# Kernel optimization log

Hardware: AMD Instinct MI355X
Metric: run time of the kernel (lower is better)

## Reference

```python
import jax, jax.numpy as jnp
import numpy as np

B, N, D, S = 4, 8, 64, 8192  # batch, heads, dim_head, seq_len


def setup_inputs() -> dict:
    key = jax.random.key(0)
    kq, kk, kv = jax.random.split(key, 3)
    q = jax.random.normal(kq, (B, N, D, S), dtype=jnp.float32)
    k = jax.random.normal(kk, (B, N, D, S), dtype=jnp.float32)
    v = jax.random.normal(kv, (B, N, D, S), dtype=jnp.float32)
    return {"q": q, "k": k, "v": v}


def reference(q, k, v):
    # q, k, v: [b, n, d, s] = [batch, heads, dim_head, seq]
    scale = q.shape[-2] ** -0.5  # dim_head^-0.5
    qs = jax.nn.softmax(q, axis=-2) * scale   # softmax over feature dim
    ks = jax.nn.softmax(k, axis=-1)           # softmax over seq dim
    # kv context: [b, n, d, d] -- avoids the O(s^2) score matrix
    context = jnp.einsum('bnis,bnjs->bnij', ks, v)
    # out: [b, n, d, s]
    return jnp.einsum('bnij,bnis->bnjs', context, qs)
```

## Files before the change

kernel.cpp:

```cpp
#include <hip/hip_runtime.h>
#include <math.h>


typedef _Float16 half8 __attribute__((ext_vector_type(8)));
typedef float floatx4 __attribute__((ext_vector_type(4)));
typedef float floatx16 __attribute__((ext_vector_type(16)));

constexpr int BHEADS = 32;
constexpr int DH     = 64;
constexpr int SEQ    = 8192;
constexpr int NCHUNK = 32;
constexpr float QSCALE = 0.125f;

__global__ __launch_bounds__(256)
void ctx_partial_kernel(const float* __restrict__ K, const float* __restrict__ V,
                        float* __restrict__ partial, float* __restrict__ Zp)
{
    const int head  = blockIdx.y;
    const int chunk = blockIdx.x;
    const int t     = threadIdx.x;
    const int lane  = t & 63;
    const int w     = t >> 6;
    const int ln    = lane & 15;
    const int q8    = lane >> 4;

    const float* kh = K + (size_t)head * DH * SEQ;
    const float* vh = V + (size_t)head * DH * SEQ;

    __shared__ __align__(16) _Float16 et[64 * 72];
    __shared__ __align__(16) _Float16 vt[64 * 72];
    __shared__ __align__(16) float zred[64 * 8];

    const int r0 = t >> 3;
    const int c0 = 8 * (t & 7);
    const int s_blk = chunk * 256;

    float4 pk[2][2], pv[2][2];
    #pragma unroll
    for (int rr = 0; rr < 2; ++rr) {
        const size_t base = (size_t)(r0 + 32 * rr) * SEQ + s_blk + c0;
        pk[rr][0] = *(const float4*)(kh + base);
        pk[rr][1] = *(const float4*)(kh + base + 4);
        pv[rr][0] = *(const float4*)(vh + base);
        pv[rr][1] = *(const float4*)(vh + base + 4);
    }

    floatx4 acc[4];
    #pragma unroll
    for (int jt = 0; jt < 4; ++jt) acc[jt] = (floatx4){0.f, 0.f, 0.f, 0.f};
    float zacc[2] = {0.f, 0.f};

    for (int ts = 0; ts < 4; ++ts) {
        #pragma unroll
        for (int rr = 0; rr < 2; ++rr) {
            const int row = r0 + 32 * rr;
            float e[8];
            e[0] = __expf(pk[rr][0].x); e[1] = __expf(pk[rr][0].y);
            e[2] = __expf(pk[rr][0].z); e[3] = __expf(pk[rr][0].w);
            e[4] = __expf(pk[rr][1].x); e[5] = __expf(pk[rr][1].y);
            e[6] = __expf(pk[rr][1].z); e[7] = __expf(pk[rr][1].w);
            zacc[rr] += e[0]+e[1]+e[2]+e[3]+e[4]+e[5]+e[6]+e[7];
            half8 he, hv;
            #pragma unroll
            for (int x = 0; x < 4; ++x) {
                he[x] = (_Float16)e[x]; he[x+4] = (_Float16)e[x+4];
            }
            hv[0] = (_Float16)pv[rr][0].x; hv[1] = (_Float16)pv[rr][0].y;
            hv[2] = (_Float16)pv[rr][0].z; hv[3] = (_Float16)pv[rr][0].w;
            hv[4] = (_Float16)pv[rr][1].x; hv[5] = (_Float16)pv[rr][1].y;
            hv[6] = (_Float16)pv[rr][1].z; hv[7] = (_Float16)pv[rr][1].w;
            *(half8*)(et + row * 72 + c0) = he;
            *(half8*)(vt + row * 72 + c0) = hv;
        }
        if (ts < 3) {
            #pragma unroll
            for (int rr = 0; rr < 2; ++rr) {
                const size_t base = (size_t)(r0 + 32 * rr) * SEQ + s_blk
                                    + (ts + 1) * 64 + c0;
                pk[rr][0] = *(const float4*)(kh + base);
                pk[rr][1] = *(const float4*)(kh + base + 4);
                pv[rr][0] = *(const float4*)(vh + base);
                pv[rr][1] = *(const float4*)(vh + base + 4);
            }
        }
        __syncthreads();
        #pragma unroll
        for (int st = 0; st < 2; ++st) {
            const half8 a = *(const half8*)(et + (16 * w + ln) * 72 + st * 32 + q8 * 8);
            #pragma unroll
            for (int jt = 0; jt < 4; ++jt) {
                const half8 b = *(const half8*)(vt + (16 * jt + ln) * 72 + st * 32 + q8 * 8);
                acc[jt] = __builtin_amdgcn_mfma_f32_16x16x32_f16(a, b, acc[jt], 0, 0, 0);
            }
        }
        __syncthreads();
    }

    float* ph = partial + (size_t)(head * NCHUNK + chunk) * DH * DH;
    #pragma unroll
    for (int jt = 0; jt < 4; ++jt) {
        #pragma unroll
        for (int rr = 0; rr < 4; ++rr) {
            const int i = 16 * w + q8 * 4 + rr;
            const int j = 16 * jt + ln;
            ph[i * DH + j] = acc[jt][rr];
        }
    }
    zred[r0 * 8 + (t & 7)] = zacc[0];
    zred[(r0 + 32) * 8 + (t & 7)] = zacc[1];
    __syncthreads();
    if (t < 64) {
        const float4 z0 = *(const float4*)(zred + t * 8);
        const float4 z1 = *(const float4*)(zred + t * 8 + 4);
        Zp[(head * NCHUNK + chunk) * DH + t] =
            z0.x + z0.y + z0.z + z0.w + z1.x + z1.y + z1.z + z1.w;
    }
}

__global__ __launch_bounds__(256)
void reduce_kernel(const float* __restrict__ partial, const float* __restrict__ Zp,
                   _Float16* __restrict__ czT)
{
    const int h  = blockIdx.x >> 2;
    const int iq = blockIdx.x & 3;
    const int t  = threadIdx.x;
    __shared__ float rz[16];

    if (t < 16) {
        float z = 0.f;
        #pragma unroll
        for (int c = 0; c < NCHUNK; ++c)
            z += Zp[(h * NCHUNK + c) * DH + 16 * iq + t];
        rz[t] = 1.0f / z;
    }
    __syncthreads();

    const int il = t >> 4;
    const int j4 = t & 15;
    const int i  = 16 * iq + il;
    const float* ph = partial + (size_t)h * NCHUNK * DH * DH;
    float4 sum = {0.f, 0.f, 0.f, 0.f};
    #pragma unroll
    for (int c = 0; c < NCHUNK; ++c) {
        const float4 p = *(const float4*)(ph + (size_t)c * DH * DH + i * DH + j4 * 4);
        sum.x += p.x; sum.y += p.y; sum.z += p.z; sum.w += p.w;
    }
    const float r = rz[il];
    _Float16* ct = czT + (size_t)h * DH * DH;
    ct[(j4 * 4 + 0) * DH + i] = (_Float16)(sum.x * r);
    ct[(j4 * 4 + 1) * DH + i] = (_Float16)(sum.y * r);
    ct[(j4 * 4 + 2) * DH + i] = (_Float16)(sum.z * r);
    ct[(j4 * 4 + 3) * DH + i] = (_Float16)(sum.w * r);
}

__global__ __launch_bounds__(256)
void out_kernel(const float* __restrict__ Q, const _Float16* __restrict__ czT,
                float* __restrict__ out)
{
    const int head = blockIdx.y;
    const int sb   = blockIdx.x;
    const int t    = threadIdx.x;
    const int lane = t & 63;
    const int w    = t >> 6;
    const int l31  = lane & 31;
    const int lh   = lane >> 5;
    const int jw   = 32 * (w & 1);
    const int sw   = 32 * (w >> 1);

    __shared__ __align__(16) float    qf[64 * 68];
    __shared__ __align__(16) _Float16 eqT[64 * 64];
    __shared__ __align__(16) float    wred[64 * 4];

    const float* qh = Q + (size_t)head * DH * SEQ;
    const int r0 = t >> 4;
    const int sc = 4 * (t & 15);
    const int s0 = sb * 128;

    float4 pq[4];
    #pragma unroll
    for (int p = 0; p < 4; ++p)
        pq[p] = *(const float4*)(qh + (size_t)(r0 + 16 * p) * SEQ + s0 + sc);

    const _Float16* ch = czT + (size_t)head * DH * DH;
    half8 afr[4];
    #pragma unroll
    for (int st = 0; st < 4; ++st)
        afr[st] = *(const half8*)(ch + (jw + l31) * DH + st * 16 + lh * 8);

    for (int r = 0; r < 2; ++r) {
        #pragma unroll
        for (int p = 0; p < 4; ++p)
            *(float4*)(qf + (r0 + 16 * p) * 68 + sc) = pq[p];
        if (r < 1) {
            #pragma unroll
            for (int p = 0; p < 4; ++p)
                pq[p] = *(const float4*)(qh + (size_t)(r0 + 16 * p) * SEQ
                                         + s0 + 64 + sc);
        }
        __syncthreads();
        {
            const int s  = t & 63;
            const int cg = t >> 6;
            float wsum = 0.f;
            #pragma unroll
            for (int h2 = 0; h2 < 2; ++h2) {
                const int cc = cg + 4 * h2;
                half8 p8;
                #pragma unroll
                for (int jj = 0; jj < 8; ++jj) {
                    const float e = __expf(qf[(8 * cc + jj) * 68 + s]);
                    wsum += e;
                    p8[jj] = (_Float16)e;
                }
                *(half8*)(eqT + s * 64 + ((cc ^ (s & 7)) * 8)) = p8;
            }
            wred[s * 4 + cg] = wsum;
        }
        __syncthreads();
        const float4 wv = *(const float4*)(wred + (sw + l31) * 4);
        const float rw = QSCALE / (wv.x + wv.y + wv.z + wv.w);
        floatx16 acc = {};
        #pragma unroll
        for (int st = 0; st < 4; ++st) {
            const int s2 = sw + l31;
            const int cc = 2 * st + lh;
            const half8 b = *(const half8*)(eqT + s2 * 64 + ((cc ^ (s2 & 7)) * 8));
            acc = __builtin_amdgcn_mfma_f32_32x32x16_f16(afr[st], b, acc, 0, 0, 0);
        }
        float* oh = out + (size_t)head * DH * SEQ + s0 + r * 64;
        #pragma unroll
        for (int rg = 0; rg < 16; ++rg) {
            const int j = jw + (rg & 3) + 8 * (rg >> 2) + 4 * lh;
            oh[(size_t)j * SEQ + sw + l31] = acc[rg] * rw;
        }
    }
}

extern "C" void kernel_launch(void* const* d_in, const int* in_sizes, int n_in,
                              void* d_out, int out_size, void* d_ws, size_t ws_size,
                              hipStream_t stream)
{
    const float* q = (const float*)d_in[0];
    const float* k = (const float*)d_in[1];
    const float* v = (const float*)d_in[2];
    float* out = (float*)d_out;

    float*    partial = (float*)d_ws;
    float*    Zp      = partial + BHEADS * NCHUNK * DH * DH;
    _Float16* czT     = (_Float16*)(Zp + BHEADS * NCHUNK * DH);

    ctx_partial_kernel<<<dim3(NCHUNK, BHEADS), 256, 0, stream>>>(k, v, partial, Zp);
    reduce_kernel<<<BHEADS * 4, 256, 0, stream>>>(partial, Zp, czT);
    out_kernel<<<dim3(64, BHEADS), 256, 0, stream>>>(q, czT, out);
}
```

Before: 237.8 us.

## Load MFMA operands directly from global memory, drop LDS staging in ctx kernel

The context-partial kernel no longer stages exp(K) and V through shared memory with barriers. Each lane loads its MFMA fragment straight from global memory into registers, double-buffered across 8 k-steps, and converts to fp16 in registers. Per-row Z sums now use wave shuffles instead of an LDS reduction. The reduce kernel is split into 4x more blocks with one scalar output per thread, and every thread recomputes its Z sum. In exchange, each V fragment is loaded redundantly by all 4 waves and the global accesses are less coalesced (32-byte segments per row).

```diff
diff --git a/kernel.cpp b/kernel.cpp
--- a/kernel.cpp
+++ b/kernel.cpp
@@ -24,76 +24,60 @@
     const int ln    = lane & 15;
     const int q8    = lane >> 4;
 
-    const float* kh = K + (size_t)head * DH * SEQ;
-    const float* vh = V + (size_t)head * DH * SEQ;
-
-    __shared__ __align__(16) _Float16 et[64 * 72];
-    __shared__ __align__(16) _Float16 vt[64 * 72];
-    __shared__ __align__(16) float zred[64 * 8];
-
-    const int r0 = t >> 3;
-    const int c0 = 8 * (t & 7);
-    const int s_blk = chunk * 256;
-
-    float4 pk[2][2], pv[2][2];
-    #pragma unroll
-    for (int rr = 0; rr < 2; ++rr) {
-        const size_t base = (size_t)(r0 + 32 * rr) * SEQ + s_blk + c0;
-        pk[rr][0] = *(const float4*)(kh + base);
-        pk[rr][1] = *(const float4*)(kh + base + 4);
-        pv[rr][0] = *(const float4*)(vh + base);
-        pv[rr][1] = *(const float4*)(vh + base + 4);
-    }
+    const int s0 = chunk * 256;
+    const float* ka = K + (size_t)head * DH * SEQ
+                        + (size_t)(16 * w + ln) * SEQ + s0 + q8 * 8;
+    const float* va = V + (size_t)head * DH * SEQ
+                        + (size_t)ln * SEQ + s0 + q8 * 8;
 
     floatx4 acc[4];
     #pragma unroll
     for (int jt = 0; jt < 4; ++jt) acc[jt] = (floatx4){0.f, 0.f, 0.f, 0.f};
-    float zacc[2] = {0.f, 0.f};
-
-    for (int ts = 0; ts < 4; ++ts) {
-        #pragma unroll
-        for (int rr = 0; rr < 2; ++rr) {
-            const int row = r0 + 32 * rr;
-            float e[8];
-            e[0] = __expf(pk[rr][0].x); e[1] = __expf(pk[rr][0].y);
-            e[2] = __expf(pk[rr][0].z); e[3] = __expf(pk[rr][0].w);
-            e[4] = __expf(pk[rr][1].x); e[5] = __expf(pk[rr][1].y);
-            e[6] = __expf(pk[rr][1].z); e[7] = __expf(pk[rr][1].w);
-            zacc[rr] += e[0]+e[1]+e[2]+e[3]+e[4]+e[5]+e[6]+e[7];
-            half8 he, hv;
-            #pragma unroll
-            for (int x = 0; x < 4; ++x) {
-                he[x] = (_Float16)e[x]; he[x+4] = (_Float16)e[x+4];
-            }
-            hv[0] = (_Float16)pv[rr][0].x; hv[1] = (_Float16)pv[rr][0].y;
-            hv[2] = (_Float16)pv[rr][0].z; hv[3] = (_Float16)pv[rr][0].w;
-            hv[4] = (_Float16)pv[rr][1].x; hv[5] = (_Float16)pv[rr][1].y;
-            hv[6] = (_Float16)pv[rr][1].z; hv[7] = (_Float16)pv[rr][1].w;
-            *(half8*)(et + row * 72 + c0) = he;
-            *(half8*)(vt + row * 72 + c0) = hv;
-        }
-        if (ts < 3) {
-            #pragma unroll
-            for (int rr = 0; rr < 2; ++rr) {
-                const size_t base = (size_t)(r0 + 32 * rr) * SEQ + s_blk
-                                    + (ts + 1) * 64 + c0;
-                pk[rr][0] = *(const float4*)(kh + base);
-                pk[rr][1] = *(const float4*)(kh + base + 4);
-                pv[rr][0] = *(const float4*)(vh + base);
-                pv[rr][1] = *(const float4*)(vh + base + 4);
-            }
-        }
-        __syncthreads();
-        #pragma unroll
-        for (int st = 0; st < 2; ++st) {
-            const half8 a = *(const half8*)(et + (16 * w + ln) * 72 + st * 32 + q8 * 8);
+    float zacc = 0.f;
+
+    float4 cak[2][2];
+    float4 cbv[2][4][2];
+
+    cak[0][0] = *(const float4*)(ka);
+    cak[0][1] = *(const float4*)(ka + 4);
+    #pragma unroll
+    for (int jt = 0; jt < 4; ++jt) {
+        cbv[0][jt][0] = *(const float4*)(va + (size_t)jt * 16 * SEQ);
+        cbv[0][jt][1] = *(const float4*)(va + (size_t)jt * 16 * SEQ + 4);
+    }
+
+    #pragma unroll
+    for (int kk = 0; kk < 8; ++kk) {
+        const int cur = kk & 1;
+        const int nxt = cur ^ 1;
+        if (kk < 7) {
+            const int off = (kk + 1) * 32;
+            cak[nxt][0] = *(const float4*)(ka + off);
+            cak[nxt][1] = *(const float4*)(ka + off + 4);
             #pragma unroll
             for (int jt = 0; jt < 4; ++jt) {
-                const half8 b = *(const half8*)(vt + (16 * jt + ln) * 72 + st * 32 + q8 * 8);
-                acc[jt] = __builtin_amdgcn_mfma_f32_16x16x32_f16(a, b, acc[jt], 0, 0, 0);
+                cbv[nxt][jt][0] = *(const float4*)(va + (size_t)jt * 16 * SEQ + off);
+                cbv[nxt][jt][1] = *(const float4*)(va + (size_t)jt * 16 * SEQ + off + 4);
             }
         }
-        __syncthreads();
+        float e[8];
+        e[0] = __expf(cak[cur][0].x); e[1] = __expf(cak[cur][0].y);
+        e[2] = __expf(cak[cur][0].z); e[3] = __expf(cak[cur][0].w);
+        e[4] = __expf(cak[cur][1].x); e[5] = __expf(cak[cur][1].y);
+        e[6] = __expf(cak[cur][1].z); e[7] = __expf(cak[cur][1].w);
+        zacc += e[0]+e[1]+e[2]+e[3]+e[4]+e[5]+e[6]+e[7];
+        half8 ah;
+        #pragma unroll
+        for (int x = 0; x < 8; ++x) ah[x] = (_Float16)e[x];
+        #pragma unroll
+        for (int jt = 0; jt < 4; ++jt) {
+            half8 bh;
+            bh[0] = (_Float16)cbv[cur][jt][0].x; bh[1] = (_Float16)cbv[cur][jt][0].y;
+            bh[2] = (_Float16)cbv[cur][jt][0].z; bh[3] = (_Float16)cbv[cur][jt][0].w;
+            bh[4] = (_Float16)cbv[cur][jt][1].x; bh[5] = (_Float16)cbv[cur][jt][1].y;
+            bh[6] = (_Float16)cbv[cur][jt][1].z; bh[7] = (_Float16)cbv[cur][jt][1].w;
+            acc[jt] = __builtin_amdgcn_mfma_f32_16x16x32_f16(ah, bh, acc[jt], 0, 0, 0);
+        }
     }
 
     float* ph = partial + (size_t)(head * NCHUNK + chunk) * DH * DH;
@@ -106,51 +90,36 @@
             ph[i * DH + j] = acc[jt][rr];
         }
     }
-    zred[r0 * 8 + (t & 7)] = zacc[0];
-    zred[(r0 + 32) * 8 + (t & 7)] = zacc[1];
-    __syncthreads();
-    if (t < 64) {
-        const float4 z0 = *(const float4*)(zred + t * 8);
-        const float4 z1 = *(const float4*)(zred + t * 8 + 4);
-        Zp[(head * NCHUNK + chunk) * DH + t] =
-            z0.x + z0.y + z0.z + z0.w + z1.x + z1.y + z1.z + z1.w;
-    }
+
+    zacc += __shfl_xor(zacc, 16);
+    zacc += __shfl_xor(zacc, 32);
+    if (lane < 16)
+        Zp[(head * NCHUNK + chunk) * DH + 16 * w + ln] = zacc;
 }
 
 __global__ __launch_bounds__(256)
 void reduce_kernel(const float* __restrict__ partial, const float* __restrict__ Zp,
                    _Float16* __restrict__ czT)
 {
-    const int h  = blockIdx.x >> 2;
-    const int iq = blockIdx.x & 3;
+    const int h  = blockIdx.x >> 4;
+    const int ig = blockIdx.x & 15;
     const int t  = threadIdx.x;
-    __shared__ float rz[16];
-
-    if (t < 16) {
-        float z = 0.f;
-        #pragma unroll
-        for (int c = 0; c < NCHUNK; ++c)
-            z += Zp[(h * NCHUNK + c) * DH + 16 * iq + t];
-        rz[t] = 1.0f / z;
-    }
-    __syncthreads();
-
-    const int il = t >> 4;
-    const int j4 = t & 15;
-    const int i  = 16 * iq + il;
-    const float* ph = partial + (size_t)h * NCHUNK * DH * DH;
-    float4 sum = {0.f, 0.f, 0.f, 0.f};
-    #pragma unroll
-    for (int c = 0; c < NCHUNK; ++c) {
-        const float4 p = *(const float4*)(ph + (size_t)c * DH * DH + i * DH + j4 * 4);
-        sum.x += p.x; sum.y += p.y; sum.z += p.z; sum.w += p.w;
-    }
-    const float r = rz[il];
-    _Float16* ct = czT + (size_t)h * DH * DH;
-    ct[(j4 * 4 + 0) * DH + i] = (_Float16)(sum.x * r);
-    ct[(j4 * 4 + 1) * DH + i] = (_Float16)(sum.y * r);
-    ct[(j4 * 4 + 2) * DH + i] = (_Float16)(sum.z * r);
-    ct[(j4 * 4 + 3) * DH + i] = (_Float16)(sum.w * r);
+    const int il = t >> 6;
+    const int j  = t & 63;
+    const int i  = 4 * ig + il;
+
+    const float* ph = partial + (size_t)h * NCHUNK * DH * DH + i * DH + j;
+    float sum = 0.f;
+    #pragma unroll
+    for (int c = 0; c < NCHUNK; ++c)
+        sum += ph[(size_t)c * DH * DH];
+
+    float z = 0.f;
+    #pragma unroll
+    for (int c = 0; c < NCHUNK; ++c)
+        z += Zp[(h * NCHUNK + c) * DH + i];
+
+    czT[(size_t)h * DH * DH + j * DH + i] = (_Float16)(sum / z);
 }
 
 __global__ __launch_bounds__(256)
@@ -250,6 +219,6 @@
     _Float16* czT     = (_Float16*)(Zp + BHEADS * NCHUNK * DH);
 
     ctx_partial_kernel<<<dim3(NCHUNK, BHEADS), 256, 0, stream>>>(k, v, partial, Zp);
-    reduce_kernel<<<BHEADS * 4, 256, 0, stream>>>(partial, Zp, czT);
+    reduce_kernel<<<BHEADS * 16, 256, 0, stream>>>(partial, Zp, czT);
     out_kernel<<<dim3(64, BHEADS), 256, 0, stream>>>(q, czT, out);
 }
```

New measurement: 241.4 us. Within noise of the previous version (+1.5%).
